# Performance work log

Measured on AMD Instinct MI355X. Metric: run time of the kernel, lower is better.

## Reference

```python
import jax, jax.numpy as jnp
import numpy as np

EPS = 1e-5
KF = 3  # kernel_field

def _layernorm(x, g, b):
    m = jnp.mean(x, axis=-1, keepdims=True)
    v = jnp.var(x, axis=-1, keepdims=True)
    return (x - m) * jax.lax.rsqrt(v + EPS) * g + b

def _sai2token(buf, W_mlp):
    # buf: [b, c, a, h, w] -> tokens [h*w, b*a, spa_dim]
    b, c, a, h, w = buf.shape
    x = buf.transpose(0, 2, 1, 3, 4).reshape(b * a, c, h, w)
    xp = jnp.pad(x, ((0, 0), (0, 0), (1, 1), (1, 1)))
    # torch F.unfold ordering: channel slowest, then kernel (i, j)
    patches = jnp.stack([xp[:, :, i:i + h, j:j + w] for i in range(KF) for j in range(KF)], axis=2)
    tok = patches.reshape(b * a, c * KF * KF, h * w).transpose(2, 0, 1)  # [hw, ba, c*9]
    return tok @ W_mlp

def _attention(x, Wqkv, Wproj, bproj, Wl, bl, Ww, bw, lamb, num_heads):
    B, N, C = x.shape
    hd = C // num_heads
    scale = hd ** -0.5
    qkv = (x @ Wqkv).reshape(B, N, 3, num_heads, hd).transpose(2, 0, 3, 1, 4)
    q, k, v = qkv[0] * scale, qkv[1], qkv[2]  # each [B, H, N, hd]
    attn = jnp.einsum('bhnd,bhmd->bhnm', q, k)
    # talking-heads mix before softmax (proj_l)
    attn = jnp.einsum('bhnm,gh->bgnm', attn, Wl) + bl[None, :, None, None]
    attn = jax.nn.softmax(attn, axis=-1)
    # talking-heads mix after softmax (proj_w)
    attn = jnp.einsum('bhnm,gh->bgnm', attn, Ww) + bw[None, :, None, None]
    # attnscale: attn_d + (attn - attn_d) * (1 + lamb_h)
    attn_d = 1.0 / N
    attn = attn_d + (attn - attn_d) * (1.0 + lamb[None, :, None, None])
    out = jnp.einsum('bhnm,bhmd->bhnd', attn, v).transpose(0, 2, 1, 3).reshape(B, N, C)
    return out @ Wproj + bproj


def setup_inputs() -> dict:
    key = jax.random.key(0)
    ks = jax.random.split(key, 20)
    b, c, a, h, w = 4, 128, 25, 32, 32
    D = 2 * c           # spa_dim = 256
    H = 8               # num_heads
    cin = c * KF * KF   # 1152
    f32 = jnp.float32
    def nrm(k, shp, s=0.02):
        return (jax.random.normal(k, shp, dtype=f32) * s)
    return {
        'buffer': jax.random.normal(ks[0], (b, c, a, h, w), dtype=f32),
        'spa_position': jax.random.normal(ks[1], (b, c, a, h, w), dtype=f32) * 0.02,
        'W_mlp': nrm(ks[2], (cin, D)),
        'g1': jnp.ones((D,), f32), 'b1': jnp.zeros((D,), f32),
        'Wqkv': nrm(ks[3], (D, 3 * D)),
        'Wproj': nrm(ks[4], (D, D)), 'bproj': jnp.zeros((D,), f32),
        'Wl': nrm(ks[5], (H, H), 0.3), 'bl': jnp.zeros((H,), f32),
        'Ww': nrm(ks[6], (H, H), 0.3), 'bw': jnp.zeros((H,), f32),
        'lamb': jnp.zeros((H,), f32),
        'g2': jnp.ones((D,), f32), 'b2': jnp.zeros((D,), f32),
        'W1': nrm(ks[7], (D, 2 * D)),
        'W2': nrm(ks[8], (2 * D, D)),
        'Wconv': nrm(ks[9], (c, D)),
    }


def reference(buffer, spa_position, W_mlp, g1, b1, Wqkv, Wproj, bproj,
              Wl, bl, Ww, bw, lamb, g2, b2, W1, W2, Wconv):
    b, c, a, h, w = buffer.shape
    num_heads = Wl.shape[0]
    # gen_mask is computed in the original forward but never used -> omitted.
    spa_token = _sai2token(buffer, W_mlp)          # [hw, ba, D]
    spa_PE = _sai2token(spa_position, W_mlp)       # [hw, ba, D]
    x = _layernorm(spa_token + spa_PE, g1, b1)
    spa_token = _attention(x, Wqkv, Wproj, bproj, Wl, bl, Ww, bw, lamb, num_heads) + spa_token
    # feed-forward: LN -> Linear(D,2D,no bias) -> ReLU -> Linear(2D,D,no bias)
    y = _layernorm(spa_token, g2, b2)
    y = jax.nn.relu(y @ W1) @ W2
    spa_token = y + spa_token
    # Token2SAI: '(h w) (b a) c -> b c a h w' then 1x1x1 Conv3d (D -> c, no bias)
    D = spa_token.shape[-1]
    buf = spa_token.reshape(h, w, b, a, D).transpose(2, 4, 3, 0, 1)  # [b, D, a, h, w]
    out = jnp.einsum('bdahw,od->boahw', buf, Wconv)
    return out
```

## Files before the change

kernel.cpp:

```cpp
#include <hip/hip_runtime.h>
#include <hip/hip_bf16.h>

typedef unsigned short u16;
typedef unsigned int u32;
typedef short bf16x8 __attribute__((ext_vector_type(8)));
typedef float f32x4 __attribute__((ext_vector_type(4)));

#define MFMA(a,b,c) __builtin_amdgcn_mfma_f32_16x16x32_bf16((a),(b),(c),0,0,0)

__device__ __forceinline__ float bf2f(u16 v) { u32 t = ((u32)v) << 16; float f; __builtin_memcpy(&f, &t, 4); return f; }
__device__ __forceinline__ u16 f2bf(float f) { u32 x; __builtin_memcpy(&x, &f, 4); u32 r = (x + 0x7FFFu + ((x >> 16) & 1u)) >> 16; return (u16)r; }
__device__ __forceinline__ float san(float v) { return (fabsf(v) < 1e30f) ? v : 0.f; }
__device__ __forceinline__ float lde(const void* p, long i, int flag) {
    return flag ? bf2f(((const u16*)p)[i]) : ((const float*)p)[i];
}

__device__ __forceinline__ bf16x8 ldfrag8(const u16* p) {
    union { bf16x8 v; uint2 q[2]; } u;
    u.q[0] = *(const uint2*)p;
    u.q[1] = *(const uint2*)(p + 4);
    return u.v;
}
__device__ __forceinline__ bf16x8 ldfrag16(const u16* p) {
    union { bf16x8 v; uint4 q; } u;
    u.q = *(const uint4*)p;
    return u.v;
}

__device__ __forceinline__ void gload16(const u16* g, u16* l) {
    __builtin_amdgcn_global_load_lds(
        (const __attribute__((address_space(1))) u16*)g,
        (__attribute__((address_space(3))) u16*)l, 16, 0, 0);
}

__global__ void detect_dtype(const u32* __restrict__ g1w, int* __restrict__ flag) {
    if (threadIdx.x == 0 && blockIdx.x == 0)
        *flag = (g1w[0] == 0x3F800000u) ? 0 : 1;
}

__global__ __launch_bounds__(256) void fill_sentinel(float* __restrict__ out, int n) {
    int i = blockIdx.x * 256 + threadIdx.x;
    if (i < n) out[i] = 2.0f;
}

__global__ __launch_bounds__(256) void prep_weights(
    const void* __restrict__ Wmlp, const void* __restrict__ Wqkv,
    const void* __restrict__ Wproj, const void* __restrict__ W1,
    const void* __restrict__ W2, const void* __restrict__ Wconv,
    const void* __restrict__ g1, const void* __restrict__ b1,
    const void* __restrict__ g2, const void* __restrict__ b2,
    const void* __restrict__ bproj, const void* __restrict__ Wl,
    const void* __restrict__ Ww, const void* __restrict__ bl,
    const void* __restrict__ bw, const void* __restrict__ lamb,
    u16* __restrict__ Wt1, u16* __restrict__ WqkvT, u16* __restrict__ WprojT,
    u16* __restrict__ W1T, u16* __restrict__ W2T, u16* __restrict__ WconvF,
    float* __restrict__ PRM, u16* __restrict__ ZEROB, const int* __restrict__ flagp)
{
    int i = blockIdx.x * 256 + threadIdx.x;
    int flag = *flagp;
    if (i < 294912) {
        int d = i / 1152, kp = i % 1152;
        int pos9 = kp >> 7, ch = kp & 127;
        Wt1[i] = f2bf(lde(Wmlp, (ch * 9 + pos9) * 256 + d, flag));
    } else if (i < 491520) {
        int j = i - 294912; int jj = j / 256, kk = j % 256;
        WqkvT[j] = f2bf(lde(Wqkv, kk * 768 + jj, flag));
    } else if (i < 557056) {
        int j = i - 491520; int jj = j / 256, kk = j % 256;
        WprojT[j] = f2bf(lde(Wproj, kk * 256 + jj, flag));
    } else if (i < 688128) {
        int j = i - 557056; int jj = j / 256, kk = j % 256;
        W1T[j] = f2bf(lde(W1, kk * 512 + jj, flag));
    } else if (i < 819200) {
        int j = i - 688128; int jj = j / 512, kk = j % 512;
        W2T[j] = f2bf(lde(W2, kk * 256 + jj, flag));
    } else if (i < 851968) {
        int j = i - 819200;
        WconvF[j] = f2bf(lde(Wconv, j, flag));
    } else if (i < 853400) {
        int idx = i - 851968;
        float v;
        if      (idx < 256)  v = lde(g1,    idx,        flag);
        else if (idx < 512)  v = lde(b1,    idx - 256,  flag);
        else if (idx < 768)  v = lde(g2,    idx - 512,  flag);
        else if (idx < 1024) v = lde(b2,    idx - 768,  flag);
        else if (idx < 1280) v = lde(bproj, idx - 1024, flag);
        else if (idx < 1344) v = lde(Wl,    idx - 1280, flag);
        else if (idx < 1408) v = lde(Ww,    idx - 1344, flag);
        else if (idx < 1416) v = lde(bl,    idx - 1408, flag);
        else if (idx < 1424) v = lde(bw,    idx - 1416, flag);
        else                 v = lde(lamb,  idx - 1424, flag);
        PRM[idx] = v;
    } else if (i < 853464) {
        ZEROB[i - 853400] = 0;
    }
}

__global__ __launch_bounds__(256) void make_tokens(
    const void* __restrict__ buf, const void* __restrict__ pos,
    u16* __restrict__ tb, u16* __restrict__ ts, const int* __restrict__ flagp)
{
    __shared__ u16 t0[64 * 66];
    __shared__ u16 t1[64 * 66];
    int flag = *flagp;
    int nba = blockIdx.z; int bb = nba / 25, aa = nba % 25;
    int ch0 = blockIdx.y * 64, p0 = blockIdx.x * 64;
    int lane = threadIdx.x & 63, grp = threadIdx.x >> 6;
    for (int cc = grp; cc < 64; cc += 4) {
        long gi = ((long)(bb * 128 + ch0 + cc) * 25 + aa) * 1024 + p0 + lane;
        float v0 = lde(buf, gi, flag);
        float v1 = lde(pos, gi, flag);
        t0[cc * 66 + lane] = f2bf(v0);
        t1[cc * 66 + lane] = f2bf(v0 + v1);
    }
    __syncthreads();
    for (int pp = grp; pp < 64; pp += 4) {
        size_t go = (size_t)(p0 + pp) * 12800 + (size_t)nba * 128 + ch0 + lane;
        tb[go] = t0[lane * 66 + pp];
        ts[go] = t1[lane * 66 + pp];
    }
}

__global__ __launch_bounds__(256) void gemm_conv(
    const u16* __restrict__ Tin, const u16* __restrict__ Wt, u16* __restrict__ C,
    const u16* __restrict__ ZB)
{
    __shared__ u16 As[128 * 64];
    __shared__ u16 Bs[128 * 64];
    const int m0 = blockIdx.y * 128, n0 = blockIdx.x * 128;
    const int tid = threadIdx.x;
    const int lane = tid & 63, wave = tid >> 6;
    const int wr = wave >> 1, wc = wave & 1;
    const int l15 = lane & 15, l4 = lane >> 4;
    const int colk = (tid & 7) * 8;
    int ys[4], xs[4];
    const u16* Ab[4];
#pragma unroll
    for (int i = 0; i < 4; ++i) {
        int row = m0 + i * 32 + (tid >> 3);
        int pp = row / 100, snb = row - pp * 100;
        ys[i] = pp >> 5; xs[i] = pp & 31;
        Ab[i] = Tin + (size_t)snb * 128 + colk;
    }
    const u16* Bg = Wt + (size_t)(n0 + (tid >> 3)) * 1152 + colk;
    u16* Asw = &As[(wave * 8) * 64];
    u16* Bsw = &Bs[(wave * 8) * 64];
    f32x4 acc[4][4] = {};

    auto stage = [&](int k0) {
        int pos9 = k0 >> 7, ch0 = k0 & 127;
        int dy = pos9 / 3 - 1, dx = pos9 % 3 - 1;
#pragma unroll
        for (int i = 0; i < 4; ++i) {
            int yy = ys[i] + dy, xx = xs[i] + dx;
            bool ok = ((unsigned)yy < 32u) && ((unsigned)xx < 32u);
            const u16* src = ok ? (Ab[i] + (size_t)(yy * 32 + xx) * 12800 + ch0) : ZB;
            gload16(src, Asw + i * 32 * 64);
            gload16(Bg + (size_t)i * 32 * 1152 + k0, Bsw + i * 32 * 64);
        }
    };

    stage(0);
    int k0 = 0;
    while (true) {
        __syncthreads();
#pragma unroll
        for (int ks = 0; ks < 2; ++ks) {
            const int koff = ks * 32 + l4 * 8;
            bf16x8 af[4], bq[4];
#pragma unroll
            for (int q = 0; q < 4; ++q) {
                af[q] = ldfrag16(&As[(wr * 64 + q * 16 + l15) * 64 + koff]);
                bq[q] = ldfrag16(&Bs[(wc * 64 + q * 16 + l15) * 64 + koff]);
            }
#pragma unroll
            for (int mi = 0; mi < 4; ++mi)
#pragma unroll
                for (int ni = 0; ni < 4; ++ni)
                    acc[mi][ni] = MFMA(af[mi], bq[ni], acc[mi][ni]);
        }
        k0 += 64;
        if (k0 >= 1152) break;
        __syncthreads();
        stage(k0);
    }
#pragma unroll
    for (int mi = 0; mi < 4; ++mi)
#pragma unroll
        for (int ni = 0; ni < 4; ++ni) {
            int col = n0 + wc * 64 + ni * 16 + l15;
#pragma unroll
            for (int r = 0; r < 4; ++r) {
                int row = m0 + wr * 64 + mi * 16 + l4 * 4 + r;
                C[(size_t)row * 256 + col] = f2bf(san(acc[mi][ni][r]));
            }
        }
}

template<int MODE>
__global__ __launch_bounds__(256) void gemm_bt(
    const u16* __restrict__ A, const u16* __restrict__ Bt, u16* __restrict__ C,
    int M, int N, int K,
    const float* __restrict__ bias, const u16* __restrict__ res,
    float* __restrict__ Cf)
{
    __shared__ u16 As[128 * 64];
    __shared__ u16 Bs[128 * 64];
    const int m0 = blockIdx.y * 128, n0 = blockIdx.x * 128;
    const int tid = threadIdx.x;
    const int lane = tid & 63, wave = tid >> 6;
    const int wr = wave >> 1, wc = wave & 1;
    const int l15 = lane & 15, l4 = lane >> 4;
    const u16* Ag = A + (size_t)(m0 + (tid >> 3)) * K + (tid & 7) * 8;
    const u16* Bg = Bt + (size_t)(n0 + (tid >> 3)) * K + (tid & 7) * 8;
    u16* Asw = &As[(wave * 8) * 64];
    u16* Bsw = &Bs[(wave * 8) * 64];
    const size_t rstep = (size_t)32 * K;
    f32x4 acc[4][4] = {};

#pragma unroll
    for (int i = 0; i < 4; ++i) {
        gload16(Ag + (size_t)i * rstep, Asw + i * 32 * 64);
        gload16(Bg + (size_t)i * rstep, Bsw + i * 32 * 64);
    }
    int k0 = 0;
    while (true) {
        __syncthreads();
#pragma unroll
        for (int ks = 0; ks < 2; ++ks) {
            const int koff = ks * 32 + l4 * 8;
            bf16x8 af[4], bq[4];
#pragma unroll
            for (int q = 0; q < 4; ++q) {
                af[q] = ldfrag16(&As[(wr * 64 + q * 16 + l15) * 64 + koff]);
                bq[q] = ldfrag16(&Bs[(wc * 64 + q * 16 + l15) * 64 + koff]);
            }
#pragma unroll
            for (int mi = 0; mi < 4; ++mi)
#pragma unroll
                for (int ni = 0; ni < 4; ++ni)
                    acc[mi][ni] = MFMA(af[mi], bq[ni], acc[mi][ni]);
        }
        k0 += 64;
        if (k0 >= K) break;
        __syncthreads();
#pragma unroll
        for (int i = 0; i < 4; ++i) {
            gload16(Ag + k0 + (size_t)i * rstep, Asw + i * 32 * 64);
            gload16(Bg + k0 + (size_t)i * rstep, Bsw + i * 32 * 64);
        }
    }
#pragma unroll
    for (int mi = 0; mi < 4; ++mi)
#pragma unroll
        for (int ni = 0; ni < 4; ++ni) {
            int col = n0 + wc * 64 + ni * 16 + l15;
#pragma unroll
            for (int r = 0; r < 4; ++r) {
                int row = m0 + wr * 64 + mi * 16 + l4 * 4 + r;
                float v = san(acc[mi][ni][r]);
                if (MODE == 0) {
                    C[(size_t)row * N + col] = f2bf(v);
                } else if (MODE == 1) {
                    v += bias[col] + bf2f(res[(size_t)row * N + col]);
                    C[(size_t)row * N + col] = f2bf(san(v));
                } else if (MODE == 2) {
                    C[(size_t)row * N + col] = f2bf(fmaxf(v, 0.f));
                } else if (MODE == 3) {
                    v += bf2f(res[(size_t)row * N + col]);
                    int pp = row / 100, nb = row % 100;
                    C[((size_t)nb * 1024 + pp) * 256 + col] = f2bf(san(v));
                } else {
                    int nb = col >> 10, pp = col & 1023;
                    int bb = nb / 25, aa = nb % 25;
                    Cf[(((size_t)bb * 128 + row) * 25 + aa) * 1024 + pp] = v;
                }
            }
        }
}

__global__ __launch_bounds__(256) void ln_kernel(
    const u16* __restrict__ in, const float* __restrict__ g,
    const float* __restrict__ b, u16* __restrict__ out)
{
    int wave = threadIdx.x >> 6, lane = threadIdx.x & 63;
    size_t row = (size_t)blockIdx.x * 4 + wave;
    const u16* rp = in + row * 256 + lane * 4;
    uint2 rv = *(const uint2*)rp;
    float x0 = bf2f(rv.x & 0xffff), x1 = bf2f(rv.x >> 16);
    float x2 = bf2f(rv.y & 0xffff), x3 = bf2f(rv.y >> 16);
    float s = x0 + x1 + x2 + x3;
    float ss = x0 * x0 + x1 * x1 + x2 * x2 + x3 * x3;
    for (int off = 32; off > 0; off >>= 1) { s += __shfl_xor(s, off); ss += __shfl_xor(ss, off); }
    float mean = s * (1.f / 256.f);
    float var = ss * (1.f / 256.f) - mean * mean;
    float inv = rsqrtf(fmaxf(var, 0.f) + 1e-5f);
    float4 gv = *(const float4*)(g + lane * 4);
    float4 bv = *(const float4*)(b + lane * 4);
    u16 o0 = f2bf(san((x0 - mean) * inv * gv.x + bv.x));
    u16 o1 = f2bf(san((x1 - mean) * inv * gv.y + bv.y));
    u16 o2 = f2bf(san((x2 - mean) * inv * gv.z + bv.z));
    u16 o3 = f2bf(san((x3 - mean) * inv * gv.w + bv.w));
    uint2 ov; ov.x = (u32)o0 | ((u32)o1 << 16); ov.y = (u32)o2 | ((u32)o3 << 16);
    *(uint2*)(out + row * 256 + lane * 4) = ov;
}

__global__ __launch_bounds__(256) void attn_fused(
    const u16* __restrict__ qkv, const float* __restrict__ prm,
    u16* __restrict__ AO)
{
    const int MSS = 104;
    const int MSV = 100;
    __shared__ u16 S4s[128 * 104];
    __shared__ u16 vT[256 * 100 + 4];
    __shared__ float cl_s[64], ww_s[64];
    __shared__ float bl_s[8], bw_s[8], lam_s[8];
    int p = blockIdx.x;
    int tid = threadIdx.x;
    int lane = tid & 63, wave = tid >> 6;
    int l15 = lane & 15, l4 = lane >> 4;
    if (tid < 64) { cl_s[tid] = prm[1280 + tid] * 0.17677669529663687f; ww_s[tid] = prm[1344 + tid]; }
    else if (tid < 72) { int j = tid - 64; bl_s[j] = prm[1408 + j]; bw_s[j] = prm[1416 + j]; lam_s[j] = prm[1424 + j]; }
    const u16* base = qkv + (size_t)p * 76800;

    {
        int mg = tid >> 5;
        int dv0 = (tid & 31) * 8;
        int rot = tid & 7;
        for (int mb = 0; mb < 100; mb += 8) {
            int m = mb + mg;
            if (m < 100) {
                union { uint4 q; u16 e[8]; } u;
                u.q = *(const uint4*)(base + 512 + (size_t)m * 768 + dv0);
#pragma unroll
                for (int j = 0; j < 8; ++j) {
                    int jj = (j + rot) & 7;
                    vT[(dv0 + jj) * MSV + m] = u.e[jj];
                }
            }
        }
        if (tid < 4) vT[256 * 100 + tid] = 0;
    }
    __syncthreads();

    for (int t = 0; t < 7; ++t) {
        int n0 = t * 16;
        int nq = n0 + l15; if (nq > 99) nq = 99;
        bf16x8 qf[8];
#pragma unroll
        for (int h = 0; h < 8; ++h)
            qf[h] = ldfrag16(base + nq * 768 + h * 32 + l4 * 8);

        for (int u = wave; u < 7; u += 4) {
            int m0 = u * 16;
            int mk = m0 + l15; if (mk > 99) mk = 99;
            f32x4 S[8];
#pragma unroll
            for (int h = 0; h < 8; ++h) {
                bf16x8 kf = ldfrag16(base + mk * 768 + 256 + h * 32 + l4 * 8);
                f32x4 z = {};
                S[h] = MFMA(qf[h], kf, z);
            }
            int mm = m0 + l15;
            if (mm < 100) {
#pragma unroll
                for (int g = 0; g < 8; ++g) {
                    float bgl = bl_s[g];
#pragma unroll
                    for (int r = 0; r < 4; ++r) {
                        float s2 = bgl;
#pragma unroll
                        for (int h = 0; h < 8; ++h) s2 += cl_s[g * 8 + h] * S[h][r];
                        s2 = fminf(fmaxf(s2, -80.f), 80.f);
                        S4s[(g * 16 + l4 * 4 + r) * MSS + mm] = f2bf(s2);
                    }
                }
            }
        }
        __syncthreads();

        {
            int row = tid >> 1, sub = tid & 1;
            u16* rp = S4s + row * MSS + sub * 52;
            float v[52];
#pragma unroll
            for (int i = 0; i < 13; ++i) {
                uint2 d = *(const uint2*)(rp + i * 4);
                v[i * 4 + 0] = bf2f((u16)(d.x & 0xffff));
                v[i * 4 + 1] = bf2f((u16)(d.x >> 16));
                v[i * 4 + 2] = bf2f((u16)(d.y & 0xffff));
                v[i * 4 + 3] = bf2f((u16)(d.y >> 16));
            }
            if (sub) { v[48] = -1e30f; v[49] = -1e30f; v[50] = -1e30f; v[51] = -1e30f; }
            float m0 = v[0], m1 = v[1], m2 = v[2], m3 = v[3];
#pragma unroll
            for (int j = 4; j < 52; j += 4) {
                m0 = fmaxf(m0, v[j]);     m1 = fmaxf(m1, v[j + 1]);
                m2 = fmaxf(m2, v[j + 2]); m3 = fmaxf(m3, v[j + 3]);
            }
            float mx = fmaxf(fmaxf(m0, m1), fmaxf(m2, m3));
            mx = fmaxf(mx, __shfl_xor(mx, 1));
            float s0 = 0.f, s1 = 0.f, s2 = 0.f, s3 = 0.f;
#pragma unroll
            for (int j = 0; j < 52; j += 4) {
                v[j]     = __expf(v[j]     - mx); s0 += v[j];
                v[j + 1] = __expf(v[j + 1] - mx); s1 += v[j + 1];
                v[j + 2] = __expf(v[j + 2] - mx); s2 += v[j + 2];
                v[j + 3] = __expf(v[j + 3] - mx); s3 += v[j + 3];
            }
            float sum = (s0 + s1) + (s2 + s3);
            sum += __shfl_xor(sum, 1);
            float inv = 1.f / sum;
#pragma unroll
            for (int i = 0; i < 13; ++i) {
                uint2 d;
                d.x = (u32)f2bf(v[i * 4 + 0] * inv) | ((u32)f2bf(v[i * 4 + 1] * inv) << 16);
                d.y = (u32)f2bf(v[i * 4 + 2] * inv) | ((u32)f2bf(v[i * 4 + 3] * inv) << 16);
                *(uint2*)(rp + i * 4) = d;
            }
        }
        __syncthreads();

        for (int idx = tid; idx < 832; idx += 256) {
            int nl = idx / 52, mc = idx - (idx / 52) * 52;
            float P0[8], P1[8];
#pragma unroll
            for (int g = 0; g < 8; ++g) {
                u32 d = *(const u32*)&S4s[(g * 16 + nl) * MSS + mc * 2];
                P0[g] = bf2f((u16)(d & 0xffff));
                P1[g] = bf2f((u16)(d >> 16));
            }
#pragma unroll
            for (int gp = 0; gp < 8; ++gp) {
                float a = bw_s[gp], b = bw_s[gp];
#pragma unroll
                for (int g = 0; g < 8; ++g) {
                    float w = ww_s[gp * 8 + g];
                    a += w * P0[g]; b += w * P1[g];
                }
                float lg = 1.f + lam_s[gp];
                a = 0.01f + (a - 0.01f) * lg;
                b = 0.01f + (b - 0.01f) * lg;
                u32 d = (u32)f2bf(san(a)) | ((u32)f2bf(san(b)) << 16);
                if (mc >= 50) d = 0;
                *(u32*)&S4s[(gp * 16 + nl) * MSS + mc * 2] = d;
            }
        }
        __syncthreads();

        {
            bf16x8 zz = {};
#pragma unroll
            for (int gi = 0; gi < 2; ++gi) {
                int g = wave * 2 + gi;
                bf16x8 pa[4];
#pragma unroll
                for (int ks = 0; ks < 3; ++ks)
                    pa[ks] = ldfrag8(&S4s[(g * 16 + l15) * MSS + ks * 32 + l4 * 8]);
                pa[3] = (l4 == 0) ? ldfrag8(&S4s[(g * 16 + l15) * MSS + 96]) : zz;
#pragma unroll
                for (int dh = 0; dh < 2; ++dh) {
                    int vd = g * 32 + dh * 16 + l15;
                    f32x4 acc = {};
#pragma unroll
                    for (int ks = 0; ks < 3; ++ks) {
                        bf16x8 vb = ldfrag8(&vT[vd * MSV + ks * 32 + l4 * 8]);
                        acc = MFMA(pa[ks], vb, acc);
                    }
                    bf16x8 vb3 = (l4 == 0) ? ldfrag8(&vT[vd * MSV + 96]) : zz;
                    acc = MFMA(pa[3], vb3, acc);
#pragma unroll
                    for (int r = 0; r < 4; ++r) {
                        int n = n0 + l4 * 4 + r;
                        if (n < 100)
                            AO[((size_t)p * 100 + n) * 256 + g * 32 + dh * 16 + l15] = f2bf(san(acc[r]));
                    }
                }
            }
        }
        __syncthreads();
    }
}

extern "C" void kernel_launch(void* const* d_in, const int* in_sizes, int n_in,
                              void* d_out, int out_size, void* d_ws, size_t ws_size,
                              hipStream_t stream) {
    (void)in_sizes; (void)n_in;
    const void* buffer  = d_in[0];
    const void* spa_pos = d_in[1];
    const void* W_mlp   = d_in[2];
    const void* g1      = d_in[3];
    const void* b1      = d_in[4];
    const void* Wqkv    = d_in[5];
    const void* Wproj   = d_in[6];
    const void* bproj   = d_in[7];
    const void* Wl      = d_in[8];
    const void* bl      = d_in[9];
    const void* Ww      = d_in[10];
    const void* bw      = d_in[11];
    const void* lamb    = d_in[12];
    const void* g2      = d_in[13];
    const void* b2      = d_in[14];
    const void* W1      = d_in[15];
    const void* W2      = d_in[16];
    const void* Wconv   = d_in[17];

    if (ws_size < 263856320ULL) {
        fill_sentinel<<<(out_size + 255) / 256, 256, 0, stream>>>((float*)d_out, out_size);
        return;
    }

    char* ws = (char*)d_ws;
    u16* TINB  = (u16*)(ws + 0);
    u16* TINS  = (u16*)(ws + 26214400);
    u16* X     = (u16*)(ws + 0);
    u16* AO    = (u16*)(ws + 0);
    u16* Y0    = (u16*)(ws + 0);
    u16* T0    = (u16*)(ws + 52428800);
    u16* SPA3  = (u16*)(ws + 52428800);
    u16* T1    = (u16*)(ws + 104857600);
    u16* QKV   = (u16*)(ws + 104857600);
    u16* SPA2  = (u16*)(ws + 104857600);
    u16* H1    = (u16*)(ws + 157286400);
    u16* WT1   = (u16*)(ws + 262144000);
    u16* WQKVT = (u16*)(ws + 262733824);
    u16* WPROJT= (u16*)(ws + 263127040);
    u16* W1T   = (u16*)(ws + 263258112);
    u16* W2T   = (u16*)(ws + 263520256);
    u16* WCONVF= (u16*)(ws + 263782400);
    float* PRM = (float*)(ws + 263847936);
    int* FLAG  = (int*)(ws + 263856128);
    u16* ZB    = (u16*)(ws + 263856192);

    detect_dtype<<<1, 64, 0, stream>>>((const u32*)g1, FLAG);
    prep_weights<<<3334, 256, 0, stream>>>(W_mlp, Wqkv, Wproj, W1, W2, Wconv,
                                           g1, b1, g2, b2, bproj, Wl, Ww, bl, bw, lamb,
                                           WT1, WQKVT, WPROJT, W1T, W2T, WCONVF, PRM, ZB, FLAG);
    make_tokens<<<dim3(16, 2, 100), 256, 0, stream>>>(buffer, spa_pos, TINB, TINS, FLAG);
    gemm_conv<<<dim3(2, 800), 256, 0, stream>>>(TINB, WT1, T0, ZB);
    gemm_conv<<<dim3(2, 800), 256, 0, stream>>>(TINS, WT1, T1, ZB);
    ln_kernel<<<25600, 256, 0, stream>>>(T1, PRM + 0, PRM + 256, X);
    gemm_bt<0><<<dim3(6, 800), 256, 0, stream>>>(X, WQKVT, QKV, 102400, 768, 256, nullptr, nullptr, nullptr);
    attn_fused<<<1024, 256, 0, stream>>>(QKV, PRM, AO);
    gemm_bt<1><<<dim3(2, 800), 256, 0, stream>>>(AO, WPROJT, SPA2, 102400, 256, 256, PRM + 1024, T0, nullptr);
    ln_kernel<<<25600, 256, 0, stream>>>(SPA2, PRM + 512, PRM + 768, Y0);
    gemm_bt<2><<<dim3(4, 800), 256, 0, stream>>>(Y0, W1T, H1, 102400, 512, 256, nullptr, nullptr, nullptr);
    gemm_bt<3><<<dim3(2, 800), 256, 0, stream>>>(H1, W2T, SPA3, 102400, 256, 512, nullptr, SPA2, nullptr);
    gemm_bt<4><<<dim3(800, 1), 256, 0, stream>>>(WCONVF, SPA3, nullptr, 128, 102400, 256, nullptr, nullptr, (float*)d_out);
}
```

Baseline: 967.1 us.

## Double attention block to 512 threads and redistribute per-stage work across eight waves

The fused attention kernel now launches 512 threads per block. Each of the seven active waves computes one QK score tile, softmax uses four threads per row, and each wave handles one head in the PV MFMA stage. Tail loads now use a half-fragment load that zero-fills its upper part, so the vT padding and the mc>=50 zeroing are removed. The aim is more parallelism and shorter per-wave serial chains inside one block per pair. The cost is lower occupancy from the larger blocks and an idle eighth wave during the score stage.

```diff
diff --git a/kernel.cpp b/kernel.cpp
--- a/kernel.cpp
+++ b/kernel.cpp
@@ -24,6 +24,12 @@
 __device__ __forceinline__ bf16x8 ldfrag16(const u16* p) {
     union { bf16x8 v; uint4 q; } u;
     u.q = *(const uint4*)p;
+    return u.v;
+}
+__device__ __forceinline__ bf16x8 ldtail(const u16* p) {
+    union { bf16x8 v; uint2 q[2]; } u;
+    u.q[0] = *(const uint2*)p;
+    u.q[1].x = 0; u.q[1].y = 0;
     return u.v;
 }
 
@@ -305,14 +311,14 @@
     *(uint2*)(out + row * 256 + lane * 4) = ov;
 }
 
-__global__ __launch_bounds__(256) void attn_fused(
+__global__ __launch_bounds__(512) void attn_fused(
     const u16* __restrict__ qkv, const float* __restrict__ prm,
     u16* __restrict__ AO)
 {
     const int MSS = 104;
     const int MSV = 100;
     __shared__ u16 S4s[128 * 104];
-    __shared__ u16 vT[256 * 100 + 4];
+    __shared__ u16 vT[256 * 100];
     __shared__ float cl_s[64], ww_s[64];
     __shared__ float bl_s[8], bw_s[8], lam_s[8];
     int p = blockIdx.x;
@@ -327,7 +333,7 @@
         int mg = tid >> 5;
         int dv0 = (tid & 31) * 8;
         int rot = tid & 7;
-        for (int mb = 0; mb < 100; mb += 8) {
+        for (int mb = 0; mb < 100; mb += 16) {
             int m = mb + mg;
             if (m < 100) {
                 union { uint4 q; u16 e[8]; } u;
@@ -339,20 +345,19 @@
                 }
             }
         }
-        if (tid < 4) vT[256 * 100 + tid] = 0;
     }
     __syncthreads();
 
     for (int t = 0; t < 7; ++t) {
         int n0 = t * 16;
-        int nq = n0 + l15; if (nq > 99) nq = 99;
-        bf16x8 qf[8];
-#pragma unroll
-        for (int h = 0; h < 8; ++h)
-            qf[h] = ldfrag16(base + nq * 768 + h * 32 + l4 * 8);
-
-        for (int u = wave; u < 7; u += 4) {
-            int m0 = u * 16;
+
+        if (wave < 7) {
+            int nq = n0 + l15; if (nq > 99) nq = 99;
+            bf16x8 qf[8];
+#pragma unroll
+            for (int h = 0; h < 8; ++h)
+                qf[h] = ldfrag16(base + nq * 768 + h * 32 + l4 * 8);
+            int m0 = wave * 16;
             int mk = m0 + l15; if (mk > 99) mk = 99;
             f32x4 S[8];
 #pragma unroll
@@ -380,48 +385,43 @@
         __syncthreads();
 
         {
-            int row = tid >> 1, sub = tid & 1;
-            u16* rp = S4s + row * MSS + sub * 52;
-            float v[52];
+            int row = tid >> 2, sub = tid & 3;
+            u32* rp32 = (u32*)(S4s + row * MSS);
+            float v[26];
 #pragma unroll
             for (int i = 0; i < 13; ++i) {
-                uint2 d = *(const uint2*)(rp + i * 4);
-                v[i * 4 + 0] = bf2f((u16)(d.x & 0xffff));
-                v[i * 4 + 1] = bf2f((u16)(d.x >> 16));
-                v[i * 4 + 2] = bf2f((u16)(d.y & 0xffff));
-                v[i * 4 + 3] = bf2f((u16)(d.y >> 16));
-            }
-            if (sub) { v[48] = -1e30f; v[49] = -1e30f; v[50] = -1e30f; v[51] = -1e30f; }
-            float m0 = v[0], m1 = v[1], m2 = v[2], m3 = v[3];
-#pragma unroll
-            for (int j = 4; j < 52; j += 4) {
-                m0 = fmaxf(m0, v[j]);     m1 = fmaxf(m1, v[j + 1]);
-                m2 = fmaxf(m2, v[j + 2]); m3 = fmaxf(m3, v[j + 3]);
-            }
-            float mx = fmaxf(fmaxf(m0, m1), fmaxf(m2, m3));
+                u32 d = rp32[sub + i * 4];
+                v[2 * i]     = bf2f((u16)(d & 0xffff));
+                v[2 * i + 1] = bf2f((u16)(d >> 16));
+            }
+            if (sub >= 2) { v[24] = -1e30f; v[25] = -1e30f; }
+            float m0 = v[0], m1 = v[1];
+#pragma unroll
+            for (int j = 2; j < 26; j += 2) {
+                m0 = fmaxf(m0, v[j]); m1 = fmaxf(m1, v[j + 1]);
+            }
+            float mx = fmaxf(m0, m1);
             mx = fmaxf(mx, __shfl_xor(mx, 1));
-            float s0 = 0.f, s1 = 0.f, s2 = 0.f, s3 = 0.f;
-#pragma unroll
-            for (int j = 0; j < 52; j += 4) {
+            mx = fmaxf(mx, __shfl_xor(mx, 2));
+            float s0 = 0.f, s1 = 0.f;
+#pragma unroll
+            for (int j = 0; j < 26; j += 2) {
                 v[j]     = __expf(v[j]     - mx); s0 += v[j];
                 v[j + 1] = __expf(v[j + 1] - mx); s1 += v[j + 1];
-                v[j + 2] = __expf(v[j + 2] - mx); s2 += v[j + 2];
-                v[j + 3] = __expf(v[j + 3] - mx); s3 += v[j + 3];
-            }
-            float sum = (s0 + s1) + (s2 + s3);
+            }
+            float sum = s0 + s1;
             sum += __shfl_xor(sum, 1);
+            sum += __shfl_xor(sum, 2);
             float inv = 1.f / sum;
 #pragma unroll
             for (int i = 0; i < 13; ++i) {
-                uint2 d;
-                d.x = (u32)f2bf(v[i * 4 + 0] * inv) | ((u32)f2bf(v[i * 4 + 1] * inv) << 16);
-                d.y = (u32)f2bf(v[i * 4 + 2] * inv) | ((u32)f2bf(v[i * 4 + 3] * inv) << 16);
-                *(uint2*)(rp + i * 4) = d;
-            }
-        }
-        __syncthreads();
-
-        for (int idx = tid; idx < 832; idx += 256) {
+                u32 d = (u32)f2bf(v[2 * i] * inv) | ((u32)f2bf(v[2 * i + 1] * inv) << 16);
+                rp32[sub + i * 4] = d;
+            }
+        }
+        __syncthreads();
+
+        for (int idx = tid; idx < 832; idx += 512) {
             int nl = idx / 52, mc = idx - (idx / 52) * 52;
             float P0[8], P1[8];
 #pragma unroll
@@ -442,7 +442,6 @@
                 a = 0.01f + (a - 0.01f) * lg;
                 b = 0.01f + (b - 0.01f) * lg;
                 u32 d = (u32)f2bf(san(a)) | ((u32)f2bf(san(b)) << 16);
-                if (mc >= 50) d = 0;
                 *(u32*)&S4s[(gp * 16 + nl) * MSS + mc * 2] = d;
             }
         }
@@ -450,31 +449,28 @@
 
         {
             bf16x8 zz = {};
-#pragma unroll
-            for (int gi = 0; gi < 2; ++gi) {
-                int g = wave * 2 + gi;
-                bf16x8 pa[4];
-#pragma unroll
-                for (int ks = 0; ks < 3; ++ks)
-                    pa[ks] = ldfrag8(&S4s[(g * 16 + l15) * MSS + ks * 32 + l4 * 8]);
-                pa[3] = (l4 == 0) ? ldfrag8(&S4s[(g * 16 + l15) * MSS + 96]) : zz;
-#pragma unroll
-                for (int dh = 0; dh < 2; ++dh) {
-                    int vd = g * 32 + dh * 16 + l15;
-                    f32x4 acc = {};
-#pragma unroll
-                    for (int ks = 0; ks < 3; ++ks) {
-                        bf16x8 vb = ldfrag8(&vT[vd * MSV + ks * 32 + l4 * 8]);
-                        acc = MFMA(pa[ks], vb, acc);
-                    }
-                    bf16x8 vb3 = (l4 == 0) ? ldfrag8(&vT[vd * MSV + 96]) : zz;
-                    acc = MFMA(pa[3], vb3, acc);
-#pragma unroll
-                    for (int r = 0; r < 4; ++r) {
-                        int n = n0 + l4 * 4 + r;
-                        if (n < 100)
-                            AO[((size_t)p * 100 + n) * 256 + g * 32 + dh * 16 + l15] = f2bf(san(acc[r]));
-                    }
+            int g = wave;
+            bf16x8 pa[4];
+#pragma unroll
+            for (int ks = 0; ks < 3; ++ks)
+                pa[ks] = ldfrag8(&S4s[(g * 16 + l15) * MSS + ks * 32 + l4 * 8]);
+            pa[3] = (l4 == 0) ? ldtail(&S4s[(g * 16 + l15) * MSS + 96]) : zz;
+#pragma unroll
+            for (int dh = 0; dh < 2; ++dh) {
+                int vd = g * 32 + dh * 16 + l15;
+                f32x4 acc = {};
+#pragma unroll
+                for (int ks = 0; ks < 3; ++ks) {
+                    bf16x8 vb = ldfrag8(&vT[vd * MSV + ks * 32 + l4 * 8]);
+                    acc = MFMA(pa[ks], vb, acc);
+                }
+                bf16x8 vb3 = (l4 == 0) ? ldtail(&vT[vd * MSV + 96]) : zz;
+                acc = MFMA(pa[3], vb3, acc);
+#pragma unroll
+                for (int r = 0; r < 4; ++r) {
+                    int n = n0 + l4 * 4 + r;
+                    if (n < 100)
+                        AO[((size_t)p * 100 + n) * 256 + g * 32 + dh * 16 + l15] = f2bf(san(acc[r]));
                 }
             }
         }
@@ -541,7 +537,7 @@
     gemm_conv<<<dim3(2, 800), 256, 0, stream>>>(TINS, WT1, T1, ZB);
     ln_kernel<<<25600, 256, 0, stream>>>(T1, PRM + 0, PRM + 256, X);
     gemm_bt<0><<<dim3(6, 800), 256, 0, stream>>>(X, WQKVT, QKV, 102400, 768, 256, nullptr, nullptr, nullptr);
-    attn_fused<<<1024, 256, 0, stream>>>(QKV, PRM, AO);
+    attn_fused<<<1024, 512, 0, stream>>>(QKV, PRM, AO);
     gemm_bt<1><<<dim3(2, 800), 256, 0, stream>>>(AO, WPROJT, SPA2, 102400, 256, 256, PRM + 1024, T0, nullptr);
     ln_kernel<<<25600, 256, 0, stream>>>(SPA2, PRM + 512, PRM + 768, Y0);
     gemm_bt<2><<<dim3(4, 800), 256, 0, stream>>>(Y0, W1T, H1, 102400, 512, 256, nullptr, nullptr, nullptr);
```

After: 905.5 us. 6.4% less time.
